# Kernel tuning notes

Hardware: AMD Instinct MI355X
Metric: run time of the kernel (lower is better)

Reference implementation:

```python
import jax, jax.numpy as jnp
import numpy as np

B, Lq, Lk, E = 4, 512, 512, 128
D = 2 * E  # input feature dim = 2*encode_size


def setup_inputs() -> dict:
    key = jax.random.key(0)
    ks = jax.random.split(key, 6)
    return {
        "query": jax.random.normal(ks[0], (B, Lq, D), jnp.float32),
        "key": jax.random.normal(ks[1], (B, Lk, D), jnp.float32),
        "value": jax.random.normal(ks[2], (B, Lq, D), jnp.float32),
        "Wc1": jax.random.normal(ks[3], (D, E), jnp.float32) / np.sqrt(D),
        "Wc2": jax.random.normal(ks[4], (D, E), jnp.float32) / np.sqrt(D),
        "vc": jax.random.normal(ks[5], (E,), jnp.float32) / np.sqrt(E),
    }


def reference(query, key, value, Wc1, Wc2, vc):
    # q: [B, Lq, E], k: [B, Lk, E]
    q = query @ Wc1
    k = key @ Wc2
    # additive (Bahdanau) scores: tanh(q + k) reduced by vc -> [B, Lk, Lq]
    sjt = jnp.einsum('blqe,e->blq', jnp.tanh(q[:, None, :, :] + k[:, :, None, :]), vc)
    atten = jax.nn.softmax(sjt, axis=2)  # softmax over Lq (dim=2), dropout p=0.0 is identity
    context = jnp.einsum('blq,bqd->bld', atten, value)  # [B, Lk, D]
    return (context, atten)
```

## Files before the change

### kernel.cpp

```cpp
#include <hip/hip_runtime.h>

#define NB 4
#define LQ 512
#define LK 512
#define EE 128
#define DD 256

__device__ __forceinline__ float fast_rcp(float x) { return __builtin_amdgcn_rcpf(x); }

__global__ __launch_bounds__(256) void proj_exp_kernel(
    const float* __restrict__ query, const float* __restrict__ key,
    const float* __restrict__ Wc1, const float* __restrict__ Wc2,
    float* __restrict__ Eq, float* __restrict__ Ek)
{
    __shared__ float in_s[8][DD];
    const int r0 = blockIdx.x * 8;
    const float* src; const float* W; float* dst; int rbase;
    if (r0 < NB * LQ) { src = query; W = Wc1; dst = Eq; rbase = r0; }
    else              { src = key;   W = Wc2; dst = Ek; rbase = r0 - NB * LQ; }
    const float* srow = src + (size_t)rbase * DD;
    #pragma unroll
    for (int i = 0; i < 8; ++i)
        ((float*)in_s)[i * 256 + threadIdx.x] = srow[i * 256 + threadIdx.x];
    __syncthreads();
    const int c  = threadIdx.x & 127;
    const int rg = threadIdx.x >> 7;
    float acc[4] = {0.f, 0.f, 0.f, 0.f};
    for (int d = 0; d < DD; d += 4) {
        const float w0 = W[(d + 0) * EE + c];
        const float w1 = W[(d + 1) * EE + c];
        const float w2 = W[(d + 2) * EE + c];
        const float w3 = W[(d + 3) * EE + c];
        #pragma unroll
        for (int i = 0; i < 4; ++i) {
            const float4 x = *(const float4*)&in_s[rg * 4 + i][d];
            acc[i] += x.x * w0 + x.y * w1 + x.z * w2 + x.w * w3;
        }
    }
    #pragma unroll
    for (int i = 0; i < 4; ++i)
        dst[(size_t)(rbase + rg * 4 + i) * EE + c] = __expf(2.0f * acc[i]);
}

__global__ __launch_bounds__(256) void atten_kernel(
    const float* __restrict__ Eq, const float* __restrict__ Ek,
    const float* __restrict__ vc, float* __restrict__ attn)
{
    __shared__ float sj_s[4][LQ];
    __shared__ float rinv_s[4];
    const int b   = blockIdx.x >> 7;
    const int lt  = blockIdx.x & 127;
    const int l0  = lt * 4;
    const int tid = threadIdx.x;
    const float* eqb = Eq + (size_t)b * LQ * EE;
    const float* ekb = Ek + ((size_t)b * LK + l0) * EE;

    float vcsum = 0.f;
    for (int e = 0; e < EE; e += 4) {
        const float4 v = *(const float4*)(vc + e);
        vcsum += (v.x + v.y) + (v.z + v.w);
    }

    float s2[2][4] = {{0.f,0.f,0.f,0.f},{0.f,0.f,0.f,0.f}};
    const float* eq0 = eqb + (size_t)tid * EE;
    const float* eq1 = eqb + (size_t)(tid + 256) * EE;
    for (int e = 0; e < EE; e += 4) {
        const float4 a0 = *(const float4*)(eq0 + e);
        const float4 a1 = *(const float4*)(eq1 + e);
        const float4 vv = *(const float4*)(vc + e);
        #pragma unroll
        for (int l = 0; l < 4; ++l) {
            const float4 kk = *(const float4*)(ekb + l * EE + e);
            s2[0][l] += vv.x * fast_rcp(a0.x * kk.x + 1.0f);
            s2[0][l] += vv.y * fast_rcp(a0.y * kk.y + 1.0f);
            s2[0][l] += vv.z * fast_rcp(a0.z * kk.z + 1.0f);
            s2[0][l] += vv.w * fast_rcp(a0.w * kk.w + 1.0f);
            s2[1][l] += vv.x * fast_rcp(a1.x * kk.x + 1.0f);
            s2[1][l] += vv.y * fast_rcp(a1.y * kk.y + 1.0f);
            s2[1][l] += vv.z * fast_rcp(a1.z * kk.z + 1.0f);
            s2[1][l] += vv.w * fast_rcp(a1.w * kk.w + 1.0f);
        }
    }
    #pragma unroll
    for (int l = 0; l < 4; ++l) {
        sj_s[l][tid]       = vcsum - 2.0f * s2[0][l];
        sj_s[l][tid + 256] = vcsum - 2.0f * s2[1][l];
    }
    __syncthreads();

    const int w = tid >> 6, lane = tid & 63;
    float m = -1e30f;
    #pragma unroll
    for (int i = 0; i < 8; ++i) m = fmaxf(m, sj_s[w][lane + 64 * i]);
    #pragma unroll
    for (int off = 32; off >= 1; off >>= 1) m = fmaxf(m, __shfl_xor(m, off));
    float Z = 0.f;
    #pragma unroll
    for (int i = 0; i < 8; ++i) {
        const float ex = __expf(sj_s[w][lane + 64 * i] - m);
        sj_s[w][lane + 64 * i] = ex;
        Z += ex;
    }
    #pragma unroll
    for (int off = 32; off >= 1; off >>= 1) Z += __shfl_xor(Z, off);
    if (lane == 0) rinv_s[w] = fast_rcp(Z);
    __syncthreads();

    #pragma unroll
    for (int qq = 0; qq < 2; ++qq) {
        const int q = tid + qq * 256;
        #pragma unroll
        for (int l = 0; l < 4; ++l)
            attn[(size_t)(b * LK + l0 + l) * LQ + q] = sj_s[l][q] * rinv_s[l];
    }
}

__global__ __launch_bounds__(256) void context_kernel(
    const float* __restrict__ attn, const float* __restrict__ value,
    float* __restrict__ ctx)
{
    const int b    = blockIdx.x >> 7;
    const int lt   = blockIdx.x & 127;
    const int row0 = b * LK + lt * 4;
    const int tid  = threadIdx.x;
    const int dth  = tid & 63;
    const int g    = tid >> 6;
    const float4* v4 = (const float4*)(value + (size_t)b * LQ * DD);
    float ac[4][4];
    #pragma unroll
    for (int l = 0; l < 4; ++l) { ac[l][0]=0.f; ac[l][1]=0.f; ac[l][2]=0.f; ac[l][3]=0.f; }
    const int q0 = g * 128;
    for (int q = q0; q < q0 + 128; ++q) {
        const float4 v = v4[(size_t)q * 64 + dth];
        float al[4];
        #pragma unroll
        for (int l = 0; l < 4; ++l)
            al[l] = attn[(size_t)(row0 + l) * LQ + q];
        #pragma unroll
        for (int l = 0; l < 4; ++l) {
            ac[l][0] += al[l] * v.x; ac[l][1] += al[l] * v.y;
            ac[l][2] += al[l] * v.z; ac[l][3] += al[l] * v.w;
        }
    }
    __shared__ float red[4][4][64][4];
    #pragma unroll
    for (int l = 0; l < 4; ++l) {
        red[g][l][dth][0] = ac[l][0]; red[g][l][dth][1] = ac[l][1];
        red[g][l][dth][2] = ac[l][2]; red[g][l][dth][3] = ac[l][3];
    }
    __syncthreads();
    const int l  = tid >> 6;
    const int dt = tid & 63;
    float4 c;
    c.x = red[0][l][dt][0] + red[1][l][dt][0] + red[2][l][dt][0] + red[3][l][dt][0];
    c.y = red[0][l][dt][1] + red[1][l][dt][1] + red[2][l][dt][1] + red[3][l][dt][1];
    c.z = red[0][l][dt][2] + red[1][l][dt][2] + red[2][l][dt][2] + red[3][l][dt][2];
    c.w = red[0][l][dt][3] + red[1][l][dt][3] + red[2][l][dt][3] + red[3][l][dt][3];
    ((float4*)ctx)[(size_t)(row0 + l) * 64 + dt] = c;
}

extern "C" void kernel_launch(void* const* d_in, const int* in_sizes, int n_in,
                              void* d_out, int out_size, void* d_ws, size_t ws_size,
                              hipStream_t stream) {
    const float* query = (const float*)d_in[0];
    const float* key   = (const float*)d_in[1];
    const float* value = (const float*)d_in[2];
    const float* Wc1   = (const float*)d_in[3];
    const float* Wc2   = (const float*)d_in[4];
    const float* vc    = (const float*)d_in[5];

    float* ctx  = (float*)d_out;
    float* attn = (float*)d_out + (size_t)NB * LK * DD;

    float* Eq = ctx;
    float* Ek = ctx + (size_t)NB * LQ * EE;

    proj_exp_kernel<<<dim3(512), dim3(256), 0, stream>>>(query, key, Wc1, Wc2, Eq, Ek);
    atten_kernel<<<dim3(NB * (LK / 4)), dim3(256), 0, stream>>>(Eq, Ek, vc, attn);
    context_kernel<<<dim3(NB * (LK / 4)), dim3(256), 0, stream>>>(attn, value, ctx);
}
```

Baseline: 132.8 us.

## Stage Eq tiles in LDS for scores and enlarge row tiles in projection/context

The attention kernel now loads Eq in 128-row chunks into padded shared memory with coalesced float4 loads. Each row is split across two half-waves over E, and the halves are combined with a shuffle. Before this, each thread read its own Eq row with strided global loads. The projection and context kernels now handle 16 and 8 rows per block, so weights and value rows are reused more, but there are fewer blocks and more registers per thread. The extra syncs per chunk and the larger LDS footprint may lower occupancy in the attention kernel.

After: 173.9 us. +31.0%, slower.

```diff
diff --git a/kernel.cpp b/kernel.cpp
--- a/kernel.cpp
+++ b/kernel.cpp
@@ -13,45 +13,49 @@
     const float* __restrict__ Wc1, const float* __restrict__ Wc2,
     float* __restrict__ Eq, float* __restrict__ Ek)
 {
-    __shared__ float in_s[8][DD];
-    const int r0 = blockIdx.x * 8;
+    __shared__ float in_s[16][DD];
+    const int r0 = blockIdx.x * 16;
     const float* src; const float* W; float* dst; int rbase;
     if (r0 < NB * LQ) { src = query; W = Wc1; dst = Eq; rbase = r0; }
     else              { src = key;   W = Wc2; dst = Ek; rbase = r0 - NB * LQ; }
-    const float* srow = src + (size_t)rbase * DD;
+    const float4* srow4 = (const float4*)(src + (size_t)rbase * DD);
     #pragma unroll
-    for (int i = 0; i < 8; ++i)
-        ((float*)in_s)[i * 256 + threadIdx.x] = srow[i * 256 + threadIdx.x];
+    for (int i = 0; i < 4; ++i)
+        ((float4*)in_s)[i * 256 + threadIdx.x] = srow4[i * 256 + threadIdx.x];
     __syncthreads();
     const int c  = threadIdx.x & 127;
     const int rg = threadIdx.x >> 7;
-    float acc[4] = {0.f, 0.f, 0.f, 0.f};
+    float acc[8] = {0,0,0,0,0,0,0,0};
     for (int d = 0; d < DD; d += 4) {
         const float w0 = W[(d + 0) * EE + c];
         const float w1 = W[(d + 1) * EE + c];
         const float w2 = W[(d + 2) * EE + c];
         const float w3 = W[(d + 3) * EE + c];
         #pragma unroll
-        for (int i = 0; i < 4; ++i) {
-            const float4 x = *(const float4*)&in_s[rg * 4 + i][d];
+        for (int i = 0; i < 8; ++i) {
+            const float4 x = *(const float4*)&in_s[rg * 8 + i][d];
             acc[i] += x.x * w0 + x.y * w1 + x.z * w2 + x.w * w3;
         }
     }
     #pragma unroll
-    for (int i = 0; i < 4; ++i)
-        dst[(size_t)(rbase + rg * 4 + i) * EE + c] = __expf(2.0f * acc[i]);
+    for (int i = 0; i < 8; ++i)
+        dst[(size_t)(rbase + rg * 8 + i) * EE + c] = __expf(2.0f * acc[i]);
 }
 
 __global__ __launch_bounds__(256) void atten_kernel(
     const float* __restrict__ Eq, const float* __restrict__ Ek,
     const float* __restrict__ vc, float* __restrict__ attn)
 {
+    __shared__ float eq_s[128][132];
     __shared__ float sj_s[4][LQ];
     __shared__ float rinv_s[4];
-    const int b   = blockIdx.x >> 7;
-    const int lt  = blockIdx.x & 127;
-    const int l0  = lt * 4;
-    const int tid = threadIdx.x;
+    const int b    = blockIdx.x >> 7;
+    const int lt   = blockIdx.x & 127;
+    const int l0   = lt * 4;
+    const int tid  = threadIdx.x;
+    const int w    = tid >> 6, lane = tid & 63;
+    const int r_lo = lane & 31;
+    const int h    = lane >> 5;
     const float* eqb = Eq + (size_t)b * LQ * EE;
     const float* ekb = Ek + ((size_t)b * LK + l0) * EE;
 
@@ -61,34 +65,42 @@
         vcsum += (v.x + v.y) + (v.z + v.w);
     }
 
-    float s2[2][4] = {{0.f,0.f,0.f,0.f},{0.f,0.f,0.f,0.f}};
-    const float* eq0 = eqb + (size_t)tid * EE;
-    const float* eq1 = eqb + (size_t)(tid + 256) * EE;
-    for (int e = 0; e < EE; e += 4) {
-        const float4 a0 = *(const float4*)(eq0 + e);
-        const float4 a1 = *(const float4*)(eq1 + e);
-        const float4 vv = *(const float4*)(vc + e);
+    for (int chunk = 0; chunk < 4; ++chunk) {
+        const int q0 = chunk * 128;
+        #pragma unroll
+        for (int i = 0; i < 16; ++i) {
+            const int idx = i * 256 + tid;
+            const int row = idx >> 5, c4 = idx & 31;
+            *(float4*)&eq_s[row][c4 * 4] =
+                *(const float4*)(eqb + (size_t)(q0 + row) * EE + c4 * 4);
+        }
+        __syncthreads();
+
+        const int myr = w * 32 + r_lo;
+        const float* myrow = &eq_s[myr][h * 64];
+        float s2[4] = {0.f, 0.f, 0.f, 0.f};
+        #pragma unroll
+        for (int e4 = 0; e4 < 16; ++e4) {
+            const int e = h * 64 + e4 * 4;
+            const float4 a  = *(const float4*)(myrow + e4 * 4);
+            const float4 vv = *(const float4*)(vc + e);
+            #pragma unroll
+            for (int l = 0; l < 4; ++l) {
+                const float4 kk = *(const float4*)(ekb + l * EE + e);
+                s2[l] += vv.x * fast_rcp(a.x * kk.x + 1.0f);
+                s2[l] += vv.y * fast_rcp(a.y * kk.y + 1.0f);
+                s2[l] += vv.z * fast_rcp(a.z * kk.z + 1.0f);
+                s2[l] += vv.w * fast_rcp(a.w * kk.w + 1.0f);
+            }
+        }
         #pragma unroll
         for (int l = 0; l < 4; ++l) {
-            const float4 kk = *(const float4*)(ekb + l * EE + e);
-            s2[0][l] += vv.x * fast_rcp(a0.x * kk.x + 1.0f);
-            s2[0][l] += vv.y * fast_rcp(a0.y * kk.y + 1.0f);
-            s2[0][l] += vv.z * fast_rcp(a0.z * kk.z + 1.0f);
-            s2[0][l] += vv.w * fast_rcp(a0.w * kk.w + 1.0f);
-            s2[1][l] += vv.x * fast_rcp(a1.x * kk.x + 1.0f);
-            s2[1][l] += vv.y * fast_rcp(a1.y * kk.y + 1.0f);
-            s2[1][l] += vv.z * fast_rcp(a1.z * kk.z + 1.0f);
-            s2[1][l] += vv.w * fast_rcp(a1.w * kk.w + 1.0f);
+            s2[l] += __shfl_xor(s2[l], 32);
+            if (h == 0) sj_s[l][q0 + myr] = vcsum - 2.0f * s2[l];
         }
+        __syncthreads();
     }
-    #pragma unroll
-    for (int l = 0; l < 4; ++l) {
-        sj_s[l][tid]       = vcsum - 2.0f * s2[0][l];
-        sj_s[l][tid + 256] = vcsum - 2.0f * s2[1][l];
-    }
-    __syncthreads();
 
-    const int w = tid >> 6, lane = tid & 63;
     float m = -1e30f;
     #pragma unroll
     for (int i = 0; i < 8; ++i) m = fmaxf(m, sj_s[w][lane + 64 * i]);
@@ -119,44 +131,47 @@
     const float* __restrict__ attn, const float* __restrict__ value,
     float* __restrict__ ctx)
 {
-    const int b    = blockIdx.x >> 7;
-    const int lt   = blockIdx.x & 127;
-    const int row0 = b * LK + lt * 4;
+    const int b    = blockIdx.x >> 6;
+    const int lt   = blockIdx.x & 63;
+    const int row0 = b * LK + lt * 8;
     const int tid  = threadIdx.x;
     const int dth  = tid & 63;
     const int g    = tid >> 6;
     const float4* v4 = (const float4*)(value + (size_t)b * LQ * DD);
-    float ac[4][4];
+    float ac[8][4];
     #pragma unroll
-    for (int l = 0; l < 4; ++l) { ac[l][0]=0.f; ac[l][1]=0.f; ac[l][2]=0.f; ac[l][3]=0.f; }
+    for (int l = 0; l < 8; ++l) { ac[l][0]=0.f; ac[l][1]=0.f; ac[l][2]=0.f; ac[l][3]=0.f; }
     const int q0 = g * 128;
     for (int q = q0; q < q0 + 128; ++q) {
         const float4 v = v4[(size_t)q * 64 + dth];
-        float al[4];
+        float al[8];
         #pragma unroll
-        for (int l = 0; l < 4; ++l)
+        for (int l = 0; l < 8; ++l)
             al[l] = attn[(size_t)(row0 + l) * LQ + q];
         #pragma unroll
-        for (int l = 0; l < 4; ++l) {
+        for (int l = 0; l < 8; ++l) {
             ac[l][0] += al[l] * v.x; ac[l][1] += al[l] * v.y;
             ac[l][2] += al[l] * v.z; ac[l][3] += al[l] * v.w;
         }
     }
-    __shared__ float red[4][4][64][4];
+    __shared__ float red[4][8][64][4];
     #pragma unroll
-    for (int l = 0; l < 4; ++l) {
+    for (int l = 0; l < 8; ++l) {
         red[g][l][dth][0] = ac[l][0]; red[g][l][dth][1] = ac[l][1];
         red[g][l][dth][2] = ac[l][2]; red[g][l][dth][3] = ac[l][3];
     }
     __syncthreads();
-    const int l  = tid >> 6;
-    const int dt = tid & 63;
-    float4 c;
-    c.x = red[0][l][dt][0] + red[1][l][dt][0] + red[2][l][dt][0] + red[3][l][dt][0];
-    c.y = red[0][l][dt][1] + red[1][l][dt][1] + red[2][l][dt][1] + red[3][l][dt][1];
-    c.z = red[0][l][dt][2] + red[1][l][dt][2] + red[2][l][dt][2] + red[3][l][dt][2];
-    c.w = red[0][l][dt][3] + red[1][l][dt][3] + red[2][l][dt][3] + red[3][l][dt][3];
-    ((float4*)ctx)[(size_t)(row0 + l) * 64 + dt] = c;
+    #pragma unroll
+    for (int j = 0; j < 2; ++j) {
+        const int l  = (tid >> 6) + j * 4;
+        const int dt = tid & 63;
+        float4 c;
+        c.x = red[0][l][dt][0] + red[1][l][dt][0] + red[2][l][dt][0] + red[3][l][dt][0];
+        c.y = red[0][l][dt][1] + red[1][l][dt][1] + red[2][l][dt][1] + red[3][l][dt][1];
+        c.z = red[0][l][dt][2] + red[1][l][dt][2] + red[2][l][dt][2] + red[3][l][dt][2];
+        c.w = red[0][l][dt][3] + red[1][l][dt][3] + red[2][l][dt][3] + red[3][l][dt][3];
+        ((float4*)ctx)[(size_t)(row0 + l) * 64 + dt] = c;
+    }
 }
 
 extern "C" void kernel_launch(void* const* d_in, const int* in_sizes, int n_in,
@@ -175,7 +190,7 @@
     float* Eq = ctx;
     float* Ek = ctx + (size_t)NB * LQ * EE;
 
-    proj_exp_kernel<<<dim3(512), dim3(256), 0, stream>>>(query, key, Wc1, Wc2, Eq, Ek);
+    proj_exp_kernel<<<dim3(256), dim3(256), 0, stream>>>(query, key, Wc1, Wc2, Eq, Ek);
     atten_kernel<<<dim3(NB * (LK / 4)), dim3(256), 0, stream>>>(Eq, Ek, vc, attn);
-    context_kernel<<<dim3(NB * (LK / 4)), dim3(256), 0, stream>>>(attn, value, ctx);
+    context_kernel<<<dim3(NB * (LK / 8)), dim3(256), 0, stream>>>(attn, value, ctx);
 }
```

## Transpose Eq layout, use 512-thread attention blocks, restructure context kernel per row

Applied to the files above, without the earlier changes.

The projection kernel now writes exp(2q) transposed ([b][e][q]), so each attention thread reads one q column with coalesced scalar loads instead of strided float4 rows. The attention kernel runs 512 threads, one per q, and merges the two half-row softmax partials through shared memory. The context kernel is rewritten so each wave owns one output row and loops over all q with float4 attention loads, which removes the shared-memory reduction. Per-thread register pressure drops, in exchange for an extra sync and a smaller context grid with longer serial loops.

After: 150.7 us. +13.5%, slower.

```diff
diff --git a/kernel.cpp b/kernel.cpp
--- a/kernel.cpp
+++ b/kernel.cpp
@@ -11,18 +11,21 @@
 __global__ __launch_bounds__(256) void proj_exp_kernel(
     const float* __restrict__ query, const float* __restrict__ key,
     const float* __restrict__ Wc1, const float* __restrict__ Wc2,
-    float* __restrict__ Eq, float* __restrict__ Ek)
+    float* __restrict__ EqT, float* __restrict__ Ek)
 {
     __shared__ float in_s[8][DD];
     const int r0 = blockIdx.x * 8;
-    const float* src; const float* W; float* dst; int rbase;
-    if (r0 < NB * LQ) { src = query; W = Wc1; dst = Eq; rbase = r0; }
-    else              { src = key;   W = Wc2; dst = Ek; rbase = r0 - NB * LQ; }
-    const float* srow = src + (size_t)rbase * DD;
+    const bool is_q = (r0 < NB * LQ);
+    const float* src = is_q ? query : key;
+    const float* W   = is_q ? Wc1   : Wc2;
+    const int rbase  = is_q ? r0    : r0 - NB * LQ;
+
+    const float4* srow4 = (const float4*)(src + (size_t)rbase * DD);
     #pragma unroll
-    for (int i = 0; i < 8; ++i)
-        ((float*)in_s)[i * 256 + threadIdx.x] = srow[i * 256 + threadIdx.x];
+    for (int i = 0; i < 2; ++i)
+        ((float4*)in_s)[i * 256 + threadIdx.x] = srow4[i * 256 + threadIdx.x];
     __syncthreads();
+
     const int c  = threadIdx.x & 127;
     const int rg = threadIdx.x >> 7;
     float acc[4] = {0.f, 0.f, 0.f, 0.f};
@@ -37,23 +40,34 @@
             acc[i] += x.x * w0 + x.y * w1 + x.z * w2 + x.w * w3;
         }
     }
-    #pragma unroll
-    for (int i = 0; i < 4; ++i)
-        dst[(size_t)(rbase + rg * 4 + i) * EE + c] = __expf(2.0f * acc[i]);
+    if (is_q) {
+        const int b    = rbase >> 9;
+        const int qloc = (rbase & 511) + rg * 4;
+        float4 o;
+        o.x = __expf(2.0f * acc[0]); o.y = __expf(2.0f * acc[1]);
+        o.z = __expf(2.0f * acc[2]); o.w = __expf(2.0f * acc[3]);
+        *(float4*)&EqT[((size_t)(b * EE + c)) * LQ + qloc] = o;
+    } else {
+        #pragma unroll
+        for (int i = 0; i < 4; ++i)
+            Ek[(size_t)(rbase + rg * 4 + i) * EE + c] = __expf(2.0f * acc[i]);
+    }
 }
 
-__global__ __launch_bounds__(256) void atten_kernel(
-    const float* __restrict__ Eq, const float* __restrict__ Ek,
+__global__ __launch_bounds__(512) void atten_kernel(
+    const float* __restrict__ EqT, const float* __restrict__ Ek,
     const float* __restrict__ vc, float* __restrict__ attn)
 {
-    __shared__ float sj_s[4][LQ];
-    __shared__ float rinv_s[4];
+    __shared__ float  sj_s[4][LQ];
+    __shared__ float2 mZ_s[4][2];
+    __shared__ float  scale_s[4][2];
     const int b   = blockIdx.x >> 7;
     const int lt  = blockIdx.x & 127;
     const int l0  = lt * 4;
     const int tid = threadIdx.x;
-    const float* eqb = Eq + (size_t)b * LQ * EE;
-    const float* ekb = Ek + ((size_t)b * LK + l0) * EE;
+    const int q   = tid;
+    const float* eqc = EqT + (size_t)b * EE * LQ + q;
+    const float* ekb = Ek  + ((size_t)b * LK + l0) * EE;
 
     float vcsum = 0.f;
     for (int e = 0; e < EE; e += 4) {
@@ -61,102 +75,83 @@
         vcsum += (v.x + v.y) + (v.z + v.w);
     }
 
-    float s2[2][4] = {{0.f,0.f,0.f,0.f},{0.f,0.f,0.f,0.f}};
-    const float* eq0 = eqb + (size_t)tid * EE;
-    const float* eq1 = eqb + (size_t)(tid + 256) * EE;
+    float s2[4] = {0.f, 0.f, 0.f, 0.f};
     for (int e = 0; e < EE; e += 4) {
-        const float4 a0 = *(const float4*)(eq0 + e);
-        const float4 a1 = *(const float4*)(eq1 + e);
+        const float a0 = eqc[(size_t)(e + 0) * LQ];
+        const float a1 = eqc[(size_t)(e + 1) * LQ];
+        const float a2 = eqc[(size_t)(e + 2) * LQ];
+        const float a3 = eqc[(size_t)(e + 3) * LQ];
         const float4 vv = *(const float4*)(vc + e);
         #pragma unroll
         for (int l = 0; l < 4; ++l) {
             const float4 kk = *(const float4*)(ekb + l * EE + e);
-            s2[0][l] += vv.x * fast_rcp(a0.x * kk.x + 1.0f);
-            s2[0][l] += vv.y * fast_rcp(a0.y * kk.y + 1.0f);
-            s2[0][l] += vv.z * fast_rcp(a0.z * kk.z + 1.0f);
-            s2[0][l] += vv.w * fast_rcp(a0.w * kk.w + 1.0f);
-            s2[1][l] += vv.x * fast_rcp(a1.x * kk.x + 1.0f);
-            s2[1][l] += vv.y * fast_rcp(a1.y * kk.y + 1.0f);
-            s2[1][l] += vv.z * fast_rcp(a1.z * kk.z + 1.0f);
-            s2[1][l] += vv.w * fast_rcp(a1.w * kk.w + 1.0f);
+            s2[l] += vv.x * fast_rcp(a0 * kk.x + 1.0f);
+            s2[l] += vv.y * fast_rcp(a1 * kk.y + 1.0f);
+            s2[l] += vv.z * fast_rcp(a2 * kk.z + 1.0f);
+            s2[l] += vv.w * fast_rcp(a3 * kk.w + 1.0f);
         }
     }
     #pragma unroll
-    for (int l = 0; l < 4; ++l) {
-        sj_s[l][tid]       = vcsum - 2.0f * s2[0][l];
-        sj_s[l][tid + 256] = vcsum - 2.0f * s2[1][l];
-    }
+    for (int l = 0; l < 4; ++l)
+        sj_s[l][q] = vcsum - 2.0f * s2[l];
     __syncthreads();
 
     const int w = tid >> 6, lane = tid & 63;
+    const int l = w & 3, h2 = w >> 2, base = h2 * 256;
     float m = -1e30f;
     #pragma unroll
-    for (int i = 0; i < 8; ++i) m = fmaxf(m, sj_s[w][lane + 64 * i]);
+    for (int i = 0; i < 4; ++i) m = fmaxf(m, sj_s[l][base + lane + 64 * i]);
     #pragma unroll
     for (int off = 32; off >= 1; off >>= 1) m = fmaxf(m, __shfl_xor(m, off));
     float Z = 0.f;
     #pragma unroll
-    for (int i = 0; i < 8; ++i) {
-        const float ex = __expf(sj_s[w][lane + 64 * i] - m);
-        sj_s[w][lane + 64 * i] = ex;
+    for (int i = 0; i < 4; ++i) {
+        const int idx = base + lane + 64 * i;
+        const float ex = __expf(sj_s[l][idx] - m);
+        sj_s[l][idx] = ex;
         Z += ex;
     }
     #pragma unroll
     for (int off = 32; off >= 1; off >>= 1) Z += __shfl_xor(Z, off);
-    if (lane == 0) rinv_s[w] = fast_rcp(Z);
+    if (lane == 0) mZ_s[l][h2] = make_float2(m, Z);
+    __syncthreads();
+    if (lane == 0) {
+        const float2 A = mZ_s[l][0], B2 = mZ_s[l][1];
+        const float M  = fmaxf(A.x, B2.x);
+        const float Zt = A.y * __expf(A.x - M) + B2.y * __expf(B2.x - M);
+        scale_s[l][h2] = __expf((h2 ? B2.x : A.x) - M) * fast_rcp(Zt);
+    }
     __syncthreads();
 
     #pragma unroll
-    for (int qq = 0; qq < 2; ++qq) {
-        const int q = tid + qq * 256;
-        #pragma unroll
-        for (int l = 0; l < 4; ++l)
-            attn[(size_t)(b * LK + l0 + l) * LQ + q] = sj_s[l][q] * rinv_s[l];
-    }
+    for (int li = 0; li < 4; ++li)
+        attn[(size_t)(b * LK + l0 + li) * LQ + q] = sj_s[li][q] * scale_s[li][q >> 8];
 }
 
-__global__ __launch_bounds__(256) void context_kernel(
+__global__ __launch_bounds__(512) void context_kernel(
     const float* __restrict__ attn, const float* __restrict__ value,
     float* __restrict__ ctx)
 {
-    const int b    = blockIdx.x >> 7;
-    const int lt   = blockIdx.x & 127;
-    const int row0 = b * LK + lt * 4;
-    const int tid  = threadIdx.x;
-    const int dth  = tid & 63;
-    const int g    = tid >> 6;
-    const float4* v4 = (const float4*)(value + (size_t)b * LQ * DD);
-    float ac[4][4];
-    #pragma unroll
-    for (int l = 0; l < 4; ++l) { ac[l][0]=0.f; ac[l][1]=0.f; ac[l][2]=0.f; ac[l][3]=0.f; }
-    const int q0 = g * 128;
-    for (int q = q0; q < q0 + 128; ++q) {
-        const float4 v = v4[(size_t)q * 64 + dth];
-        float al[4];
-        #pragma unroll
-        for (int l = 0; l < 4; ++l)
-            al[l] = attn[(size_t)(row0 + l) * LQ + q];
-        #pragma unroll
-        for (int l = 0; l < 4; ++l) {
-            ac[l][0] += al[l] * v.x; ac[l][1] += al[l] * v.y;
-            ac[l][2] += al[l] * v.z; ac[l][3] += al[l] * v.w;
-        }
+    const int b    = blockIdx.x >> 6;
+    const int lt   = blockIdx.x & 63;
+    const int w    = threadIdx.x >> 6;
+    const int lane = threadIdx.x & 63;
+    const int row  = b * LK + lt * 8 + w;
+    const float4* v4   = (const float4*)(value + (size_t)b * LQ * DD);
+    const float*  arow = attn + (size_t)row * LQ;
+    float4 ac = make_float4(0.f, 0.f, 0.f, 0.f);
+    for (int q = 0; q < LQ; q += 4) {
+        const float4 a4 = *(const float4*)(arow + q);
+        const float4 v0 = v4[(size_t)(q + 0) * 64 + lane];
+        const float4 v1 = v4[(size_t)(q + 1) * 64 + lane];
+        const float4 v2 = v4[(size_t)(q + 2) * 64 + lane];
+        const float4 v3 = v4[(size_t)(q + 3) * 64 + lane];
+        ac.x += a4.x * v0.x; ac.y += a4.x * v0.y; ac.z += a4.x * v0.z; ac.w += a4.x * v0.w;
+        ac.x += a4.y * v1.x; ac.y += a4.y * v1.y; ac.z += a4.y * v1.z; ac.w += a4.y * v1.w;
+        ac.x += a4.z * v2.x; ac.y += a4.z * v2.y; ac.z += a4.z * v2.z; ac.w += a4.z * v2.w;
+        ac.x += a4.w * v3.x; ac.y += a4.w * v3.y; ac.z += a4.w * v3.z; ac.w += a4.w * v3.w;
     }
-    __shared__ float red[4][4][64][4];
-    #pragma unroll
-    for (int l = 0; l < 4; ++l) {
-        red[g][l][dth][0] = ac[l][0]; red[g][l][dth][1] = ac[l][1];
-        red[g][l][dth][2] = ac[l][2]; red[g][l][dth][3] = ac[l][3];
-    }
-    __syncthreads();
-    const int l  = tid >> 6;
-    const int dt = tid & 63;
-    float4 c;
-    c.x = red[0][l][dt][0] + red[1][l][dt][0] + red[2][l][dt][0] + red[3][l][dt][0];
-    c.y = red[0][l][dt][1] + red[1][l][dt][1] + red[2][l][dt][1] + red[3][l][dt][1];
-    c.z = red[0][l][dt][2] + red[1][l][dt][2] + red[2][l][dt][2] + red[3][l][dt][2];
-    c.w = red[0][l][dt][3] + red[1][l][dt][3] + red[2][l][dt][3] + red[3][l][dt][3];
-    ((float4*)ctx)[(size_t)(row0 + l) * 64 + dt] = c;
+    ((float4*)ctx)[(size_t)row * 64 + lane] = ac;
 }
 
 extern "C" void kernel_launch(void* const* d_in, const int* in_sizes, int n_in,
@@ -172,10 +167,10 @@
     float* ctx  = (float*)d_out;
     float* attn = (float*)d_out + (size_t)NB * LK * DD;
 
-    float* Eq = ctx;
-    float* Ek = ctx + (size_t)NB * LQ * EE;
+    float* EqT = ctx;
+    float* Ek  = ctx + (size_t)NB * LQ * EE;
 
-    proj_exp_kernel<<<dim3(512), dim3(256), 0, stream>>>(query, key, Wc1, Wc2, Eq, Ek);
-    atten_kernel<<<dim3(NB * (LK / 4)), dim3(256), 0, stream>>>(Eq, Ek, vc, attn);
-    context_kernel<<<dim3(NB * (LK / 4)), dim3(256), 0, stream>>>(attn, value, ctx);
+    proj_exp_kernel<<<dim3(512), dim3(256), 0, stream>>>(query, key, Wc1, Wc2, EqT, Ek);
+    atten_kernel<<<dim3(NB * (LK / 4)), dim3(512), 0, stream>>>(EqT, Ek, vc, attn);
+    context_kernel<<<dim3(NB * (LK / 8)), dim3(512), 0, stream>>>(attn, value, ctx);
 }
```
